# Kernel tuning notes

Hardware: AMD Instinct MI355X
Metric: run time of the kernel (lower is better)

## Reference

```python
import jax, jax.numpy as jnp
import numpy as np

SEARCH_RANGE = 4  # max_displacement; kernel_size=1, strides=1, pad=search_range
LEAKY_SLOPE = 0.1


def setup_inputs() -> dict:
    key = jax.random.key(0)
    k1, k2 = jax.random.split(key)
    B, H, W, C = 8, 128, 128, 192
    prv = jax.random.normal(k1, (B, H, W, C), dtype=jnp.float32)
    nxt = jax.random.normal(k2, (B, H, W, C), dtype=jnp.float32)
    return {"prv": prv, "nxt": nxt}


def _cost_volume(prv, nxt, d):
    # tfa CorrelationCost with kernel_size=1: for each displacement (dy, dx) in
    # [-d, d]^2, out[b,y,x,k] = mean_c prv[b,y,x,c] * nxt[b,y+dy,x+dx,c],
    # with zero padding of nxt by d. Displacements ordered row-major (dy outer).
    B, H, W, C = prv.shape
    nxt_p = jnp.pad(nxt, ((0, 0), (d, d), (d, d), (0, 0)))
    outs = []
    for dy in range(2 * d + 1):  # fixed small set (9)
        for dx in range(2 * d + 1):
            shifted = nxt_p[:, dy:dy + H, dx:dx + W, :]  # [B,H,W,C]
            outs.append(jnp.mean(prv * shifted, axis=-1))  # [B,H,W]
    return jnp.stack(outs, axis=-1)  # [B,H,W,81]


def reference(prv, nxt):
    cv = _cost_volume(prv, nxt, SEARCH_RANGE)
    return jax.nn.leaky_relu(cv, LEAKY_SLOPE)
```

## Files before the change

### kernel.cpp

```cpp
#include <hip/hip_runtime.h>
#include <hip/hip_bf16.h>


#define B_ 8
#define H_ 128
#define W_ 128
#define C_ 192
#define ND 9
#define NDISP 81
#define HT 4
#define WT 16
#define KS 64
#define NK 3
#define BROWS 12
#define BCOLS 24
#define APIX (HT * WT)
#define BPIX (BROWS * BCOLS)
#define ASTR 65
#define BSTR 289
#define AGRN (16 * ASTR)
#define BGRN (16 * BSTR)
#define NSA 4
#define NSB 18

typedef short short8 __attribute__((ext_vector_type(8)));
typedef short short4_t __attribute__((ext_vector_type(4)));
typedef float f32x4 __attribute__((ext_vector_type(4)));

static __device__ __forceinline__ short bf1(float f) {
    __hip_bfloat16 h = __float2bfloat16(f);
    return __builtin_bit_cast(short, h);
}

static __device__ __forceinline__ short4_t cvt4(float4 v) {
    short4_t r;
    r[0] = bf1(v.x); r[1] = bf1(v.y); r[2] = bf1(v.z); r[3] = bf1(v.w);
    return r;
}

static __device__ __forceinline__ short8 cat(short4_t u, short4_t v) {
    return __builtin_shufflevector(u, v, 0, 1, 2, 3, 4, 5, 6, 7);
}

__global__ __launch_bounds__(256, 3)
void cv_mfma(const float* __restrict__ prv, const float* __restrict__ nxt,
             float* __restrict__ out) {
    __shared__ short4_t sm[AGRN + BGRN];
    short4_t* sA = sm;
    short4_t* sB = sm + AGRN;

    const int tid = threadIdx.x;
    const int w0 = blockIdx.x * WT;
    const int h0 = blockIdx.y * HT;
    const int b  = blockIdx.z;

    const int lane = tid & 63;
    const int wid  = tid >> 6;
    const int lq = lane & 15;
    const int lc = lane >> 4;

    const int tp  = tid >> 4;
    const int c16 = tid & 15;

    int aoff[NSA];
#pragma unroll
    for (int i = 0; i < NSA; ++i) {
        const int p = tp + 16 * i;
        const int r = p >> 4;
        const int pc = p & 15;
        aoff[i] = ((b * H_ + h0 + r) * W_ + w0 + pc) * C_ + c16 * 4;
    }
    int boff[NSB];
    unsigned bmask = 0;
#pragma unroll
    for (int i = 0; i < NSB; ++i) {
        const int p = tp + 16 * i;
        const int row = p / BCOLS;
        const int col = p - row * BCOLS;
        const int gh = h0 - 4 + row;
        const int gw = w0 - 4 + col;
        const bool ok = ((unsigned)gh < (unsigned)H_) && ((unsigned)gw < (unsigned)W_);
        if (ok) bmask |= (1u << i);
        boff[i] = ((b * H_ + (ok ? gh : 0)) * W_ + (ok ? gw : 0)) * C_ + c16 * 4;
    }

    f32x4 acc[ND][2];
#pragma unroll
    for (int d = 0; d < ND; ++d) {
        acc[d][0] = (f32x4){0.f, 0.f, 0.f, 0.f};
        acc[d][1] = (f32x4){0.f, 0.f, 0.f, 0.f};
    }

    for (int ks = 0; ks < NK; ++ks) {
        if (ks) __syncthreads();
        const int co = ks * KS;

        {
            float4 v[NSA];
#pragma unroll
            for (int i = 0; i < NSA; ++i)
                v[i] = *(const float4*)(prv + aoff[i] + co);
#pragma unroll
            for (int i = 0; i < NSA; ++i)
                sA[c16 * ASTR + tp + 16 * i] = cvt4(v[i]);
        }
#pragma unroll
        for (int bt = 0; bt < 3; ++bt) {
            float4 v[6];
#pragma unroll
            for (int j = 0; j < 6; ++j) {
                const int i = 6 * bt + j;
                v[j] = make_float4(0.f, 0.f, 0.f, 0.f);
                if (bmask & (1u << i))
                    v[j] = *(const float4*)(nxt + boff[i] + co);
            }
#pragma unroll
            for (int j = 0; j < 6; ++j) {
                const int i = 6 * bt + j;
                sB[c16 * BSTR + tp + 16 * i] = cvt4(v[j]);
            }
        }
        __syncthreads();

        short8 a[2];
#pragma unroll
        for (int s = 0; s < 2; ++s) {
            const int cg = 8 * s + 2 * lc;
            const int pA = wid * WT + lq;
            a[s] = cat(sA[cg * ASTR + pA], sA[(cg + 1) * ASTR + pA]);
        }
#pragma unroll
        for (int dy = 0; dy < ND; ++dy) {
            const int pp0 = (wid + dy) * BCOLS + lq;
#pragma unroll
            for (int s = 0; s < 2; ++s) {
                const int cg = 8 * s + 2 * lc;
                const short8 b0 = cat(sB[cg * BSTR + pp0],     sB[(cg + 1) * BSTR + pp0]);
                const short8 b1 = cat(sB[cg * BSTR + pp0 + 8], sB[(cg + 1) * BSTR + pp0 + 8]);
                acc[dy][0] = __builtin_amdgcn_mfma_f32_16x16x32_bf16(a[s], b0, acc[dy][0], 0, 0, 0);
                acc[dy][1] = __builtin_amdgcn_mfma_f32_16x16x32_bf16(a[s], b1, acc[dy][1], 0, 0, 0);
            }
        }
    }

    const float inv = 1.0f / (float)C_;
    const int h = h0 + wid;
    if (lc < 2) {
#pragma unroll
        for (int rg = 0; rg < 4; ++rg) {
            const int r = 4 * lc + rg;
            const int dx = lq - r;
            if (dx >= 0 && dx <= 8) {
                float* o = out + (size_t)((b * H_ + h) * W_ + w0 + r) * NDISP + dx;
#pragma unroll
                for (int dy = 0; dy < ND; ++dy) {
                    const float v = acc[dy][0][rg] * inv;
                    o[dy * ND] = v >= 0.f ? v : 0.1f * v;
                }
            }
        }
    } else {
#pragma unroll
        for (int rg = 0; rg < 4; ++rg) {
            const int r = 4 * lc + rg;
            const int dx = lq - r + 8;
            if (dx >= 0 && dx <= 8) {
                float* o = out + (size_t)((b * H_ + h) * W_ + w0 + r) * NDISP + dx;
#pragma unroll
                for (int dy = 0; dy < ND; ++dy) {
                    const float v = acc[dy][1][rg] * inv;
                    o[dy * ND] = v >= 0.f ? v : 0.1f * v;
                }
            }
        }
    }
}

extern "C" void kernel_launch(void* const* d_in, const int* in_sizes, int n_in,
                              void* d_out, int out_size, void* d_ws, size_t ws_size,
                              hipStream_t stream) {
    const float* prv = (const float*)d_in[0];
    const float* nxt = (const float*)d_in[1];
    float* out = (float*)d_out;

    dim3 grid(W_ / WT, H_ / HT, B_);
    cv_mfma<<<grid, 256, 0, stream>>>(prv, nxt, out);
}
```

Measured before the change: 81.82 us.

## Halve channel chunk to shrink LDS and raise occupancy, remap grid batch-fastest

Each channel step now covers 32 channels instead of 64, in six steps, so the shared-memory tile is about half as large and launch bounds ask for five blocks per CU instead of three. The grid is flattened to one dimension with the batch index varying fastest, which changes which tiles run at the same time and so how they share L2. The aim is more resident waves to hide global-load latency. The cost is twice as many barriers and staging rounds per block, each with less MFMA work between syncs.

```diff
diff --git a/kernel.cpp b/kernel.cpp
--- a/kernel.cpp
+++ b/kernel.cpp
@@ -10,18 +10,16 @@
 #define NDISP 81
 #define HT 4
 #define WT 16
-#define KS 64
-#define NK 3
+#define KS 32
+#define NK 6
 #define BROWS 12
 #define BCOLS 24
 #define APIX (HT * WT)
 #define BPIX (BROWS * BCOLS)
 #define ASTR 65
 #define BSTR 289
-#define AGRN (16 * ASTR)
-#define BGRN (16 * BSTR)
-#define NSA 4
-#define NSB 18
+#define NSA 2
+#define NSB 9
 
 typedef short short8 __attribute__((ext_vector_type(8)));
 typedef short short4_t __attribute__((ext_vector_type(4)));
@@ -42,46 +40,48 @@
     return __builtin_shufflevector(u, v, 0, 1, 2, 3, 4, 5, 6, 7);
 }
 
-__global__ __launch_bounds__(256, 3)
+__global__ __launch_bounds__(256, 5)
 void cv_mfma(const float* __restrict__ prv, const float* __restrict__ nxt,
              float* __restrict__ out) {
-    __shared__ short4_t sm[AGRN + BGRN];
+    __shared__ short4_t sm[8 * ASTR + 8 * BSTR];
     short4_t* sA = sm;
-    short4_t* sB = sm + AGRN;
+    short4_t* sB = sm + 8 * ASTR;
+
+    const int bid = blockIdx.x;
+    const int b   = bid & 7;
+    const int t   = bid >> 3;
+    const int w0  = (t & 7) * WT;
+    const int h0  = (t >> 3) * HT;
 
     const int tid = threadIdx.x;
-    const int w0 = blockIdx.x * WT;
-    const int h0 = blockIdx.y * HT;
-    const int b  = blockIdx.z;
-
     const int lane = tid & 63;
     const int wid  = tid >> 6;
     const int lq = lane & 15;
     const int lc = lane >> 4;
 
-    const int tp  = tid >> 4;
-    const int c16 = tid & 15;
+    const int tp = tid >> 3;
+    const int c8 = tid & 7;
 
     int aoff[NSA];
 #pragma unroll
     for (int i = 0; i < NSA; ++i) {
-        const int p = tp + 16 * i;
+        const int p = tp + 32 * i;
         const int r = p >> 4;
         const int pc = p & 15;
-        aoff[i] = ((b * H_ + h0 + r) * W_ + w0 + pc) * C_ + c16 * 4;
+        aoff[i] = ((b * H_ + h0 + r) * W_ + w0 + pc) * C_ + c8 * 4;
     }
     int boff[NSB];
     unsigned bmask = 0;
 #pragma unroll
     for (int i = 0; i < NSB; ++i) {
-        const int p = tp + 16 * i;
+        const int p = tp + 32 * i;
         const int row = p / BCOLS;
         const int col = p - row * BCOLS;
         const int gh = h0 - 4 + row;
         const int gw = w0 - 4 + col;
         const bool ok = ((unsigned)gh < (unsigned)H_) && ((unsigned)gw < (unsigned)W_);
         if (ok) bmask |= (1u << i);
-        boff[i] = ((b * H_ + (ok ? gh : 0)) * W_ + (ok ? gw : 0)) * C_ + c16 * 4;
+        boff[i] = ((b * H_ + (ok ? gh : 0)) * W_ + (ok ? gw : 0)) * C_ + c8 * 4;
     }
 
     f32x4 acc[ND][2];
@@ -96,50 +96,39 @@
         const int co = ks * KS;
 
         {
-            float4 v[NSA];
-#pragma unroll
-            for (int i = 0; i < NSA; ++i)
-                v[i] = *(const float4*)(prv + aoff[i] + co);
-#pragma unroll
-            for (int i = 0; i < NSA; ++i)
-                sA[c16 * ASTR + tp + 16 * i] = cvt4(v[i]);
+            float4 v0 = *(const float4*)(prv + aoff[0] + co);
+            float4 v1 = *(const float4*)(prv + aoff[1] + co);
+            sA[c8 * ASTR + tp]      = cvt4(v0);
+            sA[c8 * ASTR + tp + 32] = cvt4(v1);
         }
 #pragma unroll
         for (int bt = 0; bt < 3; ++bt) {
-            float4 v[6];
+            float4 v[3];
 #pragma unroll
-            for (int j = 0; j < 6; ++j) {
-                const int i = 6 * bt + j;
+            for (int j = 0; j < 3; ++j) {
+                const int i = 3 * bt + j;
                 v[j] = make_float4(0.f, 0.f, 0.f, 0.f);
                 if (bmask & (1u << i))
                     v[j] = *(const float4*)(nxt + boff[i] + co);
             }
 #pragma unroll
-            for (int j = 0; j < 6; ++j) {
-                const int i = 6 * bt + j;
-                sB[c16 * BSTR + tp + 16 * i] = cvt4(v[j]);
+            for (int j = 0; j < 3; ++j) {
+                const int i = 3 * bt + j;
+                sB[c8 * BSTR + tp + 32 * i] = cvt4(v[j]);
             }
         }
         __syncthreads();
 
-        short8 a[2];
-#pragma unroll
-        for (int s = 0; s < 2; ++s) {
-            const int cg = 8 * s + 2 * lc;
-            const int pA = wid * WT + lq;
-            a[s] = cat(sA[cg * ASTR + pA], sA[(cg + 1) * ASTR + pA]);
-        }
+        const int pA = wid * WT + lq;
+        const short8 a = cat(sA[2 * lc * ASTR + pA], sA[(2 * lc + 1) * ASTR + pA]);
+
 #pragma unroll
         for (int dy = 0; dy < ND; ++dy) {
             const int pp0 = (wid + dy) * BCOLS + lq;
-#pragma unroll
-            for (int s = 0; s < 2; ++s) {
-                const int cg = 8 * s + 2 * lc;
-                const short8 b0 = cat(sB[cg * BSTR + pp0],     sB[(cg + 1) * BSTR + pp0]);
-                const short8 b1 = cat(sB[cg * BSTR + pp0 + 8], sB[(cg + 1) * BSTR + pp0 + 8]);
-                acc[dy][0] = __builtin_amdgcn_mfma_f32_16x16x32_bf16(a[s], b0, acc[dy][0], 0, 0, 0);
-                acc[dy][1] = __builtin_amdgcn_mfma_f32_16x16x32_bf16(a[s], b1, acc[dy][1], 0, 0, 0);
-            }
+            const short8 b0 = cat(sB[2 * lc * BSTR + pp0],     sB[(2 * lc + 1) * BSTR + pp0]);
+            const short8 b1 = cat(sB[2 * lc * BSTR + pp0 + 8], sB[(2 * lc + 1) * BSTR + pp0 + 8]);
+            acc[dy][0] = __builtin_amdgcn_mfma_f32_16x16x32_bf16(a, b0, acc[dy][0], 0, 0, 0);
+            acc[dy][1] = __builtin_amdgcn_mfma_f32_16x16x32_bf16(a, b1, acc[dy][1], 0, 0, 0);
         }
     }
 
@@ -183,6 +172,5 @@
     const float* nxt = (const float*)d_in[1];
     float* out = (float*)d_out;
 
-    dim3 grid(W_ / WT, H_ / HT, B_);
-    cv_mfma<<<grid, 256, 0, stream>>>(prv, nxt, out);
+    cv_mfma<<<dim3(2048), 256, 0, stream>>>(prv, nxt, out);
 }
```

Result: slower. 129.0 us (+57.6%).
